# Performance work log

Measured on AMD Instinct MI355X. Metric: run time of the kernel, lower is better.

Reference implementation:

```python
import jax, jax.numpy as jnp
import numpy as np

TWO_PI = 2.0 * np.pi
DIST_THRESH = 0.1  # squared-distance threshold from the source


def _fourier_basis(x, y, K):
    # phase[i, l, k] = 2*pi*(k*x_i + l*y_i), k,l in 1..K, reshaped to [inchans, K*K]
    kk = jnp.arange(1, K + 1, dtype=x.dtype)  # varies along last axis (columns)
    ll = jnp.arange(1, K + 1, dtype=x.dtype)  # varies along middle axis (rows)
    phase = TWO_PI * (kk[None, None, :] * x[:, None, None]
                      + ll[None, :, None] * y[:, None, None])
    phase = phase.reshape(x.shape[0], K * K)
    return jnp.cos(phase), jnp.sin(phase)


def setup_inputs() -> dict:
    key = jax.random.key(0)
    ks = jax.random.split(key, 7)
    B, C_in, C_out, K, T = 128, 273, 270, 32, 2048
    return {
        "X": jax.random.normal(ks[0], (B, C_in, T), dtype=jnp.float32),
        "z_real": jax.random.normal(ks[1], (C_out, K * K), dtype=jnp.float32) / (32.0 * 32.0),
        "z_imag": jax.random.normal(ks[2], (C_out, K * K), dtype=jnp.float32) / (32.0 * 32.0),
        "x": jax.random.uniform(ks[3], (C_in,), dtype=jnp.float32),
        "y": jax.random.uniform(ks[4], (C_in,), dtype=jnp.float32),
        "x_drop": jax.random.uniform(ks[5], (), dtype=jnp.float32),
        "y_drop": jax.random.uniform(ks[6], (), dtype=jnp.float32),
    }


def reference(X, z_real, z_imag, x, y, x_drop, y_drop):
    K = int(np.sqrt(z_real.shape[1]))
    cos_m, sin_m = _fourier_basis(x, y, K)          # [C_in, K*K] each
    # logits over input channels: [C_out, C_in]
    a = z_real @ cos_m.T + z_imag @ sin_m.T
    # zero (not -inf) logits of channels near the drop point, as in the source
    dist2 = (x_drop - x) ** 2 + (y_drop - y) ** 2   # [C_in]
    a = jnp.where((dist2 < DIST_THRESH)[None, :], 0.0, a)
    a = jax.nn.softmax(a, axis=1)                    # [C_out, C_in]
    return jnp.einsum('oi,bit->bot', a, X)           # [B, C_out, T]
```

## Files before the change

kernel.cpp:

```cpp
#include <hip/hip_runtime.h>
#include <hip/hip_bf16.h>
#include <math.h>

typedef short s16x4 __attribute__((ext_vector_type(4)));
typedef short bf16x8 __attribute__((ext_vector_type(8)));
typedef float f32x16 __attribute__((ext_vector_type(16)));

#define C_IN 273
#define C_OUT 270
#define T_DIM 2048
#define KP 288
#define APR_STRIDE 288
#define APR_ROWS 320

#define WS_COS 0u
#define WS_SIN 1118208u
#define WS_PART 2236416u
#define WS_APERM 4743168u

#define ALD_STRIDE 592
#define A_LDS_BYTES (64 * ALD_STRIDE)
#define XBUF_BYTES 8192

__device__ __forceinline__ short f2bf(float f) {
  __hip_bfloat16 h = __float2bfloat16(f);
  short r; __builtin_memcpy(&r, &h, 2); return r;
}

__global__ void k_basis(const float* __restrict__ x, const float* __restrict__ y,
                        float* __restrict__ cosb, float* __restrict__ sinb) {
  const int i = blockIdx.x;
  const float xi = x[i], yi = y[i];
  const int base = threadIdx.x * 4;
  #pragma unroll
  for (int j = 0; j < 4; ++j) {
    const int kl = base + j;
    const float kf = (float)((kl & 31) + 1);
    const float lf = (float)((kl >> 5) + 1);
    const float ph = 6.28318530717958647692f * (kf * xi + lf * yi);
    float sn, cs;
    sincosf(ph, &sn, &cs);
    cosb[(size_t)i * 1024 + kl] = cs;
    sinb[(size_t)i * 1024 + kl] = sn;
  }
}

__global__ __launch_bounds__(256) void k_logits(const float* __restrict__ zr,
    const float* __restrict__ zi, const float* __restrict__ cosb,
    const float* __restrict__ sinb, float* __restrict__ part) {
  const int tx = threadIdx.x & 15, ty = threadIdx.x >> 4;
  const int ibase = blockIdx.x * 64 + tx * 4;
  const int obase = blockIdx.y * 64 + ty * 4;
  const int kl0 = (int)blockIdx.z * 128;
  int oc[4], ic[4];
  #pragma unroll
  for (int a = 0; a < 4; ++a) {
    oc[a] = min(obase + a, C_OUT - 1);
    ic[a] = min(ibase + a, C_IN - 1);
  }
  float acc[4][4] = {};
  for (int kl = kl0; kl < kl0 + 128; kl += 4) {
    float4 zr4[4], zi4[4], cb4[4], sb4[4];
    #pragma unroll
    for (int a = 0; a < 4; ++a) {
      zr4[a] = *(const float4*)(zr + (size_t)oc[a] * 1024 + kl);
      zi4[a] = *(const float4*)(zi + (size_t)oc[a] * 1024 + kl);
    }
    #pragma unroll
    for (int b = 0; b < 4; ++b) {
      cb4[b] = *(const float4*)(cosb + (size_t)ic[b] * 1024 + kl);
      sb4[b] = *(const float4*)(sinb + (size_t)ic[b] * 1024 + kl);
    }
    #pragma unroll
    for (int a = 0; a < 4; ++a)
      #pragma unroll
      for (int b = 0; b < 4; ++b)
        acc[a][b] += zr4[a].x * cb4[b].x + zr4[a].y * cb4[b].y
                   + zr4[a].z * cb4[b].z + zr4[a].w * cb4[b].w
                   + zi4[a].x * sb4[b].x + zi4[a].y * sb4[b].y
                   + zi4[a].z * sb4[b].z + zi4[a].w * sb4[b].w;
  }
  #pragma unroll
  for (int a = 0; a < 4; ++a)
    #pragma unroll
    for (int b = 0; b < 4; ++b) {
      const int o = obase + a, i = ibase + b;
      if (o < C_OUT && i < C_IN)
        part[((size_t)blockIdx.z * 272 + o) * 288 + i] = acc[a][b];
    }
}

__global__ __launch_bounds__(256) void k_softmax(const float* __restrict__ part,
    const float* __restrict__ x, const float* __restrict__ y,
    const float* __restrict__ xdp, const float* __restrict__ ydp,
    __hip_bfloat16* __restrict__ aperm) {
  const int o = blockIdx.x;
  const int tid = threadIdx.x;
  if (o >= C_OUT) {
    for (int s = tid; s < KP; s += 256)
      aperm[(size_t)o * APR_STRIDE + s] = __float2bfloat16(0.f);
    return;
  }
  __shared__ float red[8];
  const float xd = xdp[0], yd = ydp[0];
  const int i0 = tid, i1 = tid + 256;
  float v0, v1 = 0.f;
  {
    float s = 0.f;
    #pragma unroll
    for (int c = 0; c < 8; ++c) s += part[((size_t)c * 272 + o) * 288 + i0];
    const float dx = xd - x[i0], dy = yd - y[i0];
    v0 = (dx * dx + dy * dy < 0.1f) ? 0.f : s;
  }
  const bool has1 = (i1 < C_IN);
  if (has1) {
    float s = 0.f;
    #pragma unroll
    for (int c = 0; c < 8; ++c) s += part[((size_t)c * 272 + o) * 288 + i1];
    const float dx = xd - x[i1], dy = yd - y[i1];
    v1 = (dx * dx + dy * dy < 0.1f) ? 0.f : s;
  }
  float mv = has1 ? fmaxf(v0, v1) : v0;
  #pragma unroll
  for (int off = 32; off >= 1; off >>= 1) mv = fmaxf(mv, __shfl_down(mv, off));
  if ((tid & 63) == 0) red[tid >> 6] = mv;
  __syncthreads();
  const float M = fmaxf(fmaxf(red[0], red[1]), fmaxf(red[2], red[3]));
  const float e0 = expf(v0 - M);
  const float e1 = has1 ? expf(v1 - M) : 0.f;
  float sv = e0 + e1;
  #pragma unroll
  for (int off = 32; off >= 1; off >>= 1) sv += __shfl_down(sv, off);
  __syncthreads();
  if ((tid & 63) == 0) red[4 + (tid >> 6)] = sv;
  __syncthreads();
  const float S = red[4] + red[5] + red[6] + red[7];
  const float inv = 1.0f / S;
  {
    const int s = (i0 & ~3) | ((i0 & 3) ^ ((i0 >> 2) & 3));
    aperm[(size_t)o * APR_STRIDE + s] = __float2bfloat16(e0 * inv);
  }
  if (i1 < KP) {
    const int s = (i1 & ~3) | ((i1 & 3) ^ ((i1 >> 2) & 3));
    aperm[(size_t)o * APR_STRIDE + s] = __float2bfloat16(has1 ? e1 * inv : 0.f);
  }
}

__device__ __forceinline__ void load_chunk(const float* __restrict__ Xb, int ch,
                                           int t_base, int tid, float4 (&r)[4]) {
  const int k4 = tid & 7, t4 = tid >> 3;
  const int t = t_base + t4 * 4;
  #pragma unroll
  for (int rr = 0; rr < 4; ++rr) {
    const int i = ch * 32 + k4 * 4 + rr;
    float4 v = make_float4(0.f, 0.f, 0.f, 0.f);
    if (i < C_IN) v = *(const float4*)(Xb + (size_t)i * T_DIM + t);
    r[rr] = v;
  }
}

__device__ __forceinline__ void write_chunk(char* __restrict__ xb, int tid,
                                            const float4 (&r)[4]) {
  const int k4 = tid & 7, t4 = tid >> 3;
  const int tb = t4 >> 2, c4 = t4 & 3;
  #pragma unroll
  for (int rr = 0; rr < 4; ++rr) {
    const int j = rr ^ (k4 & 3);
    s16x4 p;
    p[0] = f2bf(r[rr].x); p[1] = f2bf(r[rr].y);
    p[2] = f2bf(r[rr].z); p[3] = f2bf(r[rr].w);
    *(s16x4*)(xb + (k4 * 8 + tb) * 128 + j * 32 + c4 * 8) = p;
  }
}

__global__ __launch_bounds__(256) void k_gemm(const float* __restrict__ X,
    const __hip_bfloat16* __restrict__ aperm, float* __restrict__ out) {
  __shared__ __align__(16) char smem[A_LDS_BYTES + 2 * XBUF_BYTES];
  const int tid = threadIdx.x;
  const int lane = tid & 63, w = tid >> 6;
  const int o_base = blockIdx.y * 64;
  const int t_base = blockIdx.x * 128;
  const float* Xb = X + (size_t)blockIdx.z * C_IN * T_DIM;

  {
    const int row = tid >> 2, q = tid & 3;
    const float4* src = (const float4*)((const char*)(aperm + (size_t)(o_base + row) * APR_STRIDE) + q * 144);
    float4* dst = (float4*)(smem + row * ALD_STRIDE + q * 144);
    #pragma unroll
    for (int v = 0; v < 9; ++v) dst[v] = src[v];
  }

  f32x16 acc[2] = {};
  const unsigned smem_u = (unsigned)(unsigned long long)(uintptr_t)smem;
  const unsigned xlds0 = smem_u + A_LDS_BYTES;
  const int lg = lane >> 4, l16 = lane & 15, l32 = lane & 31, lh = lane >> 5;
  const unsigned bconst = (unsigned)((lg >> 1) * 2048 + (lg & 1) * 128 + w * 256 + l16 * 8);

  char* xb0 = smem + A_LDS_BYTES;
  char* xb1 = smem + A_LDS_BYTES + XBUF_BYTES;

  float4 rA[4], rB[4];
  load_chunk(Xb, 0, t_base, tid, rA);
  load_chunk(Xb, 1, t_base, tid, rB);
  write_chunk(xb0, tid, rA);
  __syncthreads();

  #define COMPUTE(CH, BUFSEL)                                                      \
    {                                                                              \
      const unsigned xb = xlds0 + (BUFSEL) * XBUF_BYTES + bconst;                  \
      const char* arow0 = smem + l32 * ALD_STRIDE + ((CH) * 32) * 2 + lh * 16;     \
      _Pragma("unroll")                                                            \
      for (int kk = 0; kk < 32; kk += 16) {                                        \
        bf16x8 A0 = *(const bf16x8*)(arow0 + kk * 2);                              \
        bf16x8 A1 = *(const bf16x8*)(arow0 + 32 * ALD_STRIDE + kk * 2);            \
        s16x4 t0, t1;                                                              \
        const unsigned a0 = xb + kk * 256;                                         \
        asm volatile("ds_read_b64_tr_b16 %0, %1" : "=v"(t0) : "v"(a0));            \
        asm volatile("ds_read_b64_tr_b16 %0, %1 offset:1024" : "=v"(t1) : "v"(a0));\
        asm volatile("s_waitcnt lgkmcnt(0)" ::: "memory");                         \
        __builtin_amdgcn_sched_barrier(0);                                         \
        bf16x8 B0;                                                                 \
        B0[0] = t0[0]; B0[1] = t0[1]; B0[2] = t0[2]; B0[3] = t0[3];                \
        B0[4] = t1[0]; B0[5] = t1[1]; B0[6] = t1[2]; B0[7] = t1[3];                \
        acc[0] = __builtin_amdgcn_mfma_f32_32x32x16_bf16(A0, B0, acc[0], 0, 0, 0); \
        acc[1] = __builtin_amdgcn_mfma_f32_32x32x16_bf16(A1, B0, acc[1], 0, 0, 0); \
      }                                                                            \
    }

  for (int ch = 0; ch < 9; ch += 2) {
    if (ch + 2 < 9) load_chunk(Xb, ch + 2, t_base, tid, rA);
    COMPUTE(ch, 0)
    if (ch + 1 < 9) write_chunk(xb1, tid, rB);
    __syncthreads();
    if (ch + 1 < 9) {
      if (ch + 3 < 9) load_chunk(Xb, ch + 3, t_base, tid, rB);
      COMPUTE(ch + 1, 1)
      if (ch + 2 < 9) write_chunk(xb0, tid, rA);
      __syncthreads();
    }
  }
  #undef COMPUTE

  float* outb = out + (size_t)blockIdx.z * C_OUT * T_DIM;
  #pragma unroll
  for (int m = 0; m < 2; ++m)
    #pragma unroll
    for (int r = 0; r < 16; ++r) {
      const int o = o_base + m * 32 + (r & 3) + 8 * (r >> 2) + 4 * lh;
      if (o < C_OUT) {
        const int t = t_base + w * 32 + l32;
        outb[(size_t)o * T_DIM + t] = acc[m][r];
      }
    }
}

extern "C" void kernel_launch(void* const* d_in, const int* in_sizes, int n_in,
                              void* d_out, int out_size, void* d_ws, size_t ws_size,
                              hipStream_t stream) {
  const float* X  = (const float*)d_in[0];
  const float* zr = (const float*)d_in[1];
  const float* zi = (const float*)d_in[2];
  const float* x  = (const float*)d_in[3];
  const float* y  = (const float*)d_in[4];
  const float* xd = (const float*)d_in[5];
  const float* yd = (const float*)d_in[6];
  float* out = (float*)d_out;
  char* ws = (char*)d_ws;
  float* cosb = (float*)(ws + WS_COS);
  float* sinb = (float*)(ws + WS_SIN);
  float* part = (float*)(ws + WS_PART);
  __hip_bfloat16* aperm = (__hip_bfloat16*)(ws + WS_APERM);

  k_basis<<<dim3(273), dim3(256), 0, stream>>>(x, y, cosb, sinb);
  k_logits<<<dim3(5, 5, 8), dim3(256), 0, stream>>>(zr, zi, cosb, sinb, part);
  k_softmax<<<dim3(APR_ROWS), dim3(256), 0, stream>>>(part, x, y, xd, yd, aperm);
  k_gemm<<<dim3(16, 5, 128), dim3(256), 0, stream>>>(X, aperm, out);
}
```

Baseline: 335.7 us.

## Pre-transpose X to bf16 MFMA-ready layout and use register-only GEMM

Adds a k_trans kernel that converts X from fp32 into a bf16, k-slice-major layout matching the MFMA B-operand. The attention matrix is also written in a k-slice-tiled layout. The GEMM then loads both operands straight from global memory into registers with a 3-deep software prefetch and no LDS or barriers, and each block covers 96 output rows. The intent is to remove LDS staging, transpose reads and sync overhead from the GEMM. The cost is an extra pass that reads X in fp32 and writes it back as bf16, which adds HBM traffic and a kernel launch.

```diff
diff --git a/kernel.cpp b/kernel.cpp
--- a/kernel.cpp
+++ b/kernel.cpp
@@ -10,17 +10,15 @@
 #define C_OUT 270
 #define T_DIM 2048
 #define KP 288
-#define APR_STRIDE 288
-#define APR_ROWS 320
-
-#define WS_COS 0u
-#define WS_SIN 1118208u
-#define WS_PART 2236416u
-#define WS_APERM 4743168u
-
-#define ALD_STRIDE 592
-#define A_LDS_BYTES (64 * ALD_STRIDE)
-#define XBUF_BYTES 8192
+#define NKS 18
+
+#define XT_KS_STRIDE 65536u
+#define XT_PER_B 1179648u
+#define WS2_COS   150994944u
+#define WS2_SIN   152113152u
+#define WS2_PART  153231360u
+#define WS2_APERM 155738112u
+#define APR2_KS_STRIDE 9216u
 
 __device__ __forceinline__ short f2bf(float f) {
   __hip_bfloat16 h = __float2bfloat16(f);
@@ -93,12 +91,12 @@
 __global__ __launch_bounds__(256) void k_softmax(const float* __restrict__ part,
     const float* __restrict__ x, const float* __restrict__ y,
     const float* __restrict__ xdp, const float* __restrict__ ydp,
-    __hip_bfloat16* __restrict__ aperm) {
+    __hip_bfloat16* __restrict__ ap2) {
   const int o = blockIdx.x;
   const int tid = threadIdx.x;
   if (o >= C_OUT) {
     for (int s = tid; s < KP; s += 256)
-      aperm[(size_t)o * APR_STRIDE + s] = __float2bfloat16(0.f);
+      ap2[(size_t)((s >> 4) * 288 + o) * 16 + (s & 15)] = __float2bfloat16(0.f);
     return;
   }
   __shared__ float red[8];
@@ -136,121 +134,96 @@
   __syncthreads();
   const float S = red[4] + red[5] + red[6] + red[7];
   const float inv = 1.0f / S;
-  {
-    const int s = (i0 & ~3) | ((i0 & 3) ^ ((i0 >> 2) & 3));
-    aperm[(size_t)o * APR_STRIDE + s] = __float2bfloat16(e0 * inv);
-  }
-  if (i1 < KP) {
-    const int s = (i1 & ~3) | ((i1 & 3) ^ ((i1 >> 2) & 3));
-    aperm[(size_t)o * APR_STRIDE + s] = __float2bfloat16(has1 ? e1 * inv : 0.f);
-  }
-}
-
-__device__ __forceinline__ void load_chunk(const float* __restrict__ Xb, int ch,
-                                           int t_base, int tid, float4 (&r)[4]) {
-  const int k4 = tid & 7, t4 = tid >> 3;
-  const int t = t_base + t4 * 4;
-  #pragma unroll
-  for (int rr = 0; rr < 4; ++rr) {
-    const int i = ch * 32 + k4 * 4 + rr;
-    float4 v = make_float4(0.f, 0.f, 0.f, 0.f);
-    if (i < C_IN) v = *(const float4*)(Xb + (size_t)i * T_DIM + t);
-    r[rr] = v;
-  }
-}
-
-__device__ __forceinline__ void write_chunk(char* __restrict__ xb, int tid,
-                                            const float4 (&r)[4]) {
-  const int k4 = tid & 7, t4 = tid >> 3;
-  const int tb = t4 >> 2, c4 = t4 & 3;
-  #pragma unroll
-  for (int rr = 0; rr < 4; ++rr) {
-    const int j = rr ^ (k4 & 3);
-    s16x4 p;
-    p[0] = f2bf(r[rr].x); p[1] = f2bf(r[rr].y);
-    p[2] = f2bf(r[rr].z); p[3] = f2bf(r[rr].w);
-    *(s16x4*)(xb + (k4 * 8 + tb) * 128 + j * 32 + c4 * 8) = p;
-  }
-}
-
-__global__ __launch_bounds__(256) void k_gemm(const float* __restrict__ X,
-    const __hip_bfloat16* __restrict__ aperm, float* __restrict__ out) {
-  __shared__ __align__(16) char smem[A_LDS_BYTES + 2 * XBUF_BYTES];
+  ap2[(size_t)((i0 >> 4) * 288 + o) * 16 + (i0 & 15)] = __float2bfloat16(e0 * inv);
+  if (i1 < KP)
+    ap2[(size_t)((i1 >> 4) * 288 + o) * 16 + (i1 & 15)] =
+        __float2bfloat16(has1 ? e1 * inv : 0.f);
+}
+
+__global__ __launch_bounds__(256) void k_trans(const float* __restrict__ X,
+                                               char* __restrict__ Xt) {
+  __shared__ __align__(16) char lds[64 * 592];
+  const int tid = threadIdx.x;
+  const int t0 = blockIdx.x * 64;
+  const int b = blockIdx.y;
+  const float* Xb = X + (size_t)b * C_IN * T_DIM;
+  const int tt = tid & 63, ig = tid >> 6;
+  #pragma unroll 4
+  for (int p = 0; p < 36; ++p) {
+    const int i = p * 8 + ig * 2;
+    const float v0 = (i < C_IN) ? Xb[(size_t)i * T_DIM + t0 + tt] : 0.f;
+    const float v1 = (i + 1 < C_IN) ? Xb[(size_t)(i + 1) * T_DIM + t0 + tt] : 0.f;
+    const unsigned pk = (unsigned)(unsigned short)f2bf(v0)
+                      | ((unsigned)(unsigned short)f2bf(v1) << 16);
+    *(unsigned*)(lds + tt * 592 + i * 2) = pk;
+  }
+  __syncthreads();
+  char* XtB = Xt + (size_t)b * XT_PER_B;
+  #pragma unroll
+  for (int j = 0; j < 5; ++j) {
+    const int item = j * 256 + tid;
+    if (item < NKS * 64) {
+      const int tt2 = item & 63, ks = item >> 6;
+      const char* src = lds + tt2 * 592 + ks * 32;
+      char* dst = XtB + (size_t)ks * XT_KS_STRIDE + (size_t)(t0 + tt2) * 32;
+      *(float4*)(dst)      = *(const float4*)(src);
+      *(float4*)(dst + 16) = *(const float4*)(src + 16);
+    }
+  }
+}
+
+__global__ __launch_bounds__(256) void k_gemm3(const __hip_bfloat16* __restrict__ ap2,
+    const char* __restrict__ Xt, float* __restrict__ out) {
   const int tid = threadIdx.x;
   const int lane = tid & 63, w = tid >> 6;
-  const int o_base = blockIdx.y * 64;
-  const int t_base = blockIdx.x * 128;
-  const float* Xb = X + (size_t)blockIdx.z * C_IN * T_DIM;
-
-  {
-    const int row = tid >> 2, q = tid & 3;
-    const float4* src = (const float4*)((const char*)(aperm + (size_t)(o_base + row) * APR_STRIDE) + q * 144);
-    float4* dst = (float4*)(smem + row * ALD_STRIDE + q * 144);
-    #pragma unroll
-    for (int v = 0; v < 9; ++v) dst[v] = src[v];
-  }
-
-  f32x16 acc[2] = {};
-  const unsigned smem_u = (unsigned)(unsigned long long)(uintptr_t)smem;
-  const unsigned xlds0 = smem_u + A_LDS_BYTES;
-  const int lg = lane >> 4, l16 = lane & 15, l32 = lane & 31, lh = lane >> 5;
-  const unsigned bconst = (unsigned)((lg >> 1) * 2048 + (lg & 1) * 128 + w * 256 + l16 * 8);
-
-  char* xb0 = smem + A_LDS_BYTES;
-  char* xb1 = smem + A_LDS_BYTES + XBUF_BYTES;
-
-  float4 rA[4], rB[4];
-  load_chunk(Xb, 0, t_base, tid, rA);
-  load_chunk(Xb, 1, t_base, tid, rB);
-  write_chunk(xb0, tid, rA);
-  __syncthreads();
-
-  #define COMPUTE(CH, BUFSEL)                                                      \
-    {                                                                              \
-      const unsigned xb = xlds0 + (BUFSEL) * XBUF_BYTES + bconst;                  \
-      const char* arow0 = smem + l32 * ALD_STRIDE + ((CH) * 32) * 2 + lh * 16;     \
-      _Pragma("unroll")                                                            \
-      for (int kk = 0; kk < 32; kk += 16) {                                        \
-        bf16x8 A0 = *(const bf16x8*)(arow0 + kk * 2);                              \
-        bf16x8 A1 = *(const bf16x8*)(arow0 + 32 * ALD_STRIDE + kk * 2);            \
-        s16x4 t0, t1;                                                              \
-        const unsigned a0 = xb + kk * 256;                                         \
-        asm volatile("ds_read_b64_tr_b16 %0, %1" : "=v"(t0) : "v"(a0));            \
-        asm volatile("ds_read_b64_tr_b16 %0, %1 offset:1024" : "=v"(t1) : "v"(a0));\
-        asm volatile("s_waitcnt lgkmcnt(0)" ::: "memory");                         \
-        __builtin_amdgcn_sched_barrier(0);                                         \
-        bf16x8 B0;                                                                 \
-        B0[0] = t0[0]; B0[1] = t0[1]; B0[2] = t0[2]; B0[3] = t0[3];                \
-        B0[4] = t1[0]; B0[5] = t1[1]; B0[6] = t1[2]; B0[7] = t1[3];                \
-        acc[0] = __builtin_amdgcn_mfma_f32_32x32x16_bf16(A0, B0, acc[0], 0, 0, 0); \
-        acc[1] = __builtin_amdgcn_mfma_f32_32x32x16_bf16(A1, B0, acc[1], 0, 0, 0); \
-      }                                                                            \
-    }
-
-  for (int ch = 0; ch < 9; ch += 2) {
-    if (ch + 2 < 9) load_chunk(Xb, ch + 2, t_base, tid, rA);
-    COMPUTE(ch, 0)
-    if (ch + 1 < 9) write_chunk(xb1, tid, rB);
-    __syncthreads();
-    if (ch + 1 < 9) {
-      if (ch + 3 < 9) load_chunk(Xb, ch + 3, t_base, tid, rB);
-      COMPUTE(ch + 1, 1)
-      if (ch + 2 < 9) write_chunk(xb0, tid, rA);
-      __syncthreads();
-    }
-  }
-  #undef COMPUTE
-
-  float* outb = out + (size_t)blockIdx.z * C_OUT * T_DIM;
-  #pragma unroll
-  for (int m = 0; m < 2; ++m)
+  const int l32 = lane & 31, lh = lane >> 5;
+  const int ob = blockIdx.x;
+  const int tb = blockIdx.y;
+  const int b  = blockIdx.z;
+
+  const int tblk = tb * 4 + w;
+  const char* Bbase = Xt + (size_t)b * XT_PER_B + tblk * 1024 + l32 * 32 + lh * 16;
+  const char* Abase = (const char*)ap2 + (ob * 96 + l32) * 32 + lh * 16;
+
+  f32x16 acc[3] = {};
+  bf16x8 Bf[3], Af[3][3];
+
+  Bf[0]    = *(const bf16x8*)(Bbase);
+  Af[0][0] = *(const bf16x8*)(Abase);
+  Af[0][1] = *(const bf16x8*)(Abase + 1024);
+  Af[0][2] = *(const bf16x8*)(Abase + 2048);
+  Bf[1]    = *(const bf16x8*)(Bbase + XT_KS_STRIDE);
+  Af[1][0] = *(const bf16x8*)(Abase + APR2_KS_STRIDE);
+  Af[1][1] = *(const bf16x8*)(Abase + APR2_KS_STRIDE + 1024);
+  Af[1][2] = *(const bf16x8*)(Abase + APR2_KS_STRIDE + 2048);
+  __builtin_amdgcn_sched_barrier(0);
+
+  #pragma unroll
+  for (int ks = 0; ks < NKS; ++ks) {
+    const int cur = ks % 3;
+    if (ks + 2 < NKS) {
+      const int nxt = (ks + 2) % 3;
+      Bf[nxt]    = *(const bf16x8*)(Bbase + (size_t)(ks + 2) * XT_KS_STRIDE);
+      Af[nxt][0] = *(const bf16x8*)(Abase + (ks + 2) * APR2_KS_STRIDE);
+      Af[nxt][1] = *(const bf16x8*)(Abase + (ks + 2) * APR2_KS_STRIDE + 1024);
+      Af[nxt][2] = *(const bf16x8*)(Abase + (ks + 2) * APR2_KS_STRIDE + 2048);
+    }
+    __builtin_amdgcn_sched_barrier(0);
+    acc[0] = __builtin_amdgcn_mfma_f32_32x32x16_bf16(Af[cur][0], Bf[cur], acc[0], 0, 0, 0);
+    acc[1] = __builtin_amdgcn_mfma_f32_32x32x16_bf16(Af[cur][1], Bf[cur], acc[1], 0, 0, 0);
+    acc[2] = __builtin_amdgcn_mfma_f32_32x32x16_bf16(Af[cur][2], Bf[cur], acc[2], 0, 0, 0);
+    __builtin_amdgcn_sched_barrier(0);
+  }
+
+  const int t = tblk * 32 + l32;
+  float* outb = out + (size_t)b * C_OUT * T_DIM;
+  #pragma unroll
+  for (int mi = 0; mi < 3; ++mi)
     #pragma unroll
     for (int r = 0; r < 16; ++r) {
-      const int o = o_base + m * 32 + (r & 3) + 8 * (r >> 2) + 4 * lh;
-      if (o < C_OUT) {
-        const int t = t_base + w * 32 + l32;
-        outb[(size_t)o * T_DIM + t] = acc[m][r];
-      }
+      const int o = ob * 96 + mi * 32 + (r & 3) + 8 * (r >> 2) + 4 * lh;
+      if (o < C_OUT)
+        outb[(size_t)o * T_DIM + t] = acc[mi][r];
     }
 }
 
@@ -266,13 +239,16 @@
   const float* yd = (const float*)d_in[6];
   float* out = (float*)d_out;
   char* ws = (char*)d_ws;
-  float* cosb = (float*)(ws + WS_COS);
-  float* sinb = (float*)(ws + WS_SIN);
-  float* part = (float*)(ws + WS_PART);
-  __hip_bfloat16* aperm = (__hip_bfloat16*)(ws + WS_APERM);
+
+  float* cosb = (float*)(ws + WS2_COS);
+  float* sinb = (float*)(ws + WS2_SIN);
+  float* part = (float*)(ws + WS2_PART);
+  __hip_bfloat16* ap2 = (__hip_bfloat16*)(ws + WS2_APERM);
+  char* Xt = ws;
 
   k_basis<<<dim3(273), dim3(256), 0, stream>>>(x, y, cosb, sinb);
   k_logits<<<dim3(5, 5, 8), dim3(256), 0, stream>>>(zr, zi, cosb, sinb, part);
-  k_softmax<<<dim3(APR_ROWS), dim3(256), 0, stream>>>(part, x, y, xd, yd, aperm);
-  k_gemm<<<dim3(16, 5, 128), dim3(256), 0, stream>>>(X, aperm, out);
-}
+  k_softmax<<<dim3(KP), dim3(256), 0, stream>>>(part, x, y, xd, yd, ap2);
+  k_trans<<<dim3(32, 128), dim3(256), 0, stream>>>(X, Xt);
+  k_gemm3<<<dim3(3, 16, 128), dim3(256), 0, stream>>>(ap2, Xt, out);
+}
```

Result: slower. 395.1 us (+17.7%).
